# Optimization experiments

Measured on AMD Instinct MI355X. Metric: run time of the kernel, lower is better.

The kernel has to match this reference:

```python
import jax, jax.numpy as jnp
import numpy as np

B, H, S, D = 2, 16, 2048, 128


def setup_inputs() -> dict:
    key = jax.random.key(0)
    kq, kk, kv = jax.random.split(key, 3)
    q = jax.random.normal(kq, (B, H, S, D), dtype=jnp.float32)
    k = jax.random.normal(kk, (B, H, S, D), dtype=jnp.float32)
    v = jax.random.normal(kv, (B, H, S, D), dtype=jnp.float32)
    return {"q": q, "k": k, "v": v}


def reference(q, k, v):
    # cp_size == 1 path: causal scaled dot-product attention.
    # Identical math to the ring online-softmax accumulation collapsed to one step.
    d = q.shape[-1]
    scale = d ** -0.5
    scores = jnp.einsum("bhsd,bhtd->bhst", q, k) * scale  # (B,H,S,S)
    s = scores.shape[-1]
    causal_mask = jnp.tril(jnp.ones((s, s), dtype=bool))  # (S,S)
    scores = jnp.where(causal_mask, scores, -jnp.inf)
    probs = jax.nn.softmax(scores, axis=-1)
    return jnp.einsum("bhst,bhtd->bhsd", probs, v)
```

## Files before the change

### kernel.cpp

```cpp
#include <hip/hip_runtime.h>
#include <hip/hip_bf16.h>

constexpr int Bb = 2, Hh = 16, Ss = 2048, Dd = 128;
constexpr int BM = 64, BN = 64;
constexpr int NQT = Ss / BM;
constexpr float SCALE = 0.088388347648318447f * 1.4426950408889634f;

constexpr int KSTRIDE = 272;
constexpr int VSTRIDE = 144;

typedef __attribute__((ext_vector_type(8))) short bf16x8;
typedef __attribute__((ext_vector_type(4))) float f32x4;
typedef __attribute__((ext_vector_type(4))) int int4v;

__device__ __forceinline__ unsigned bfbits(float f) {
  union { float f; unsigned u; } v; v.f = f;
  return v.u + 0x7FFFu + ((v.u >> 16) & 1u);
}
__device__ __forceinline__ unsigned pkbf(float lo, float hi) {
#if __has_builtin(__builtin_amdgcn_cvt_pk_bf16_f32)
  typedef __attribute__((ext_vector_type(2))) __bf16 bf16x2;
  bf16x2 r = __builtin_amdgcn_cvt_pk_bf16_f32(lo, hi);
  return __builtin_bit_cast(unsigned, r);
#else
  return __builtin_amdgcn_perm(bfbits(hi), bfbits(lo), 0x07060302u);
#endif
}
__device__ __forceinline__ float exp2fast(float x) {
#if __has_builtin(__builtin_amdgcn_exp2f)
  return __builtin_amdgcn_exp2f(x);
#else
  return exp2f(x);
#endif
}
__device__ __forceinline__ float fcomp(float4 f, int j) {
  return j == 0 ? f.x : (j == 1 ? f.y : (j == 2 ? f.z : f.w));
}

__global__ __launch_bounds__(256, 3)
void fa_fwd_kernel(const float* __restrict__ q, const float* __restrict__ k,
                   const float* __restrict__ v, float* __restrict__ out) {
  __shared__ __align__(16) char Klds[BN * KSTRIDE];
  __shared__ __align__(16) char Vlds[Dd * VSTRIDE];

  const int tid = threadIdx.x;
  const int wave = tid >> 6, lane = tid & 63, quad = lane >> 4, l16 = lane & 15;
  const int bid = blockIdx.x;
  const int bh = bid & 31;
  const int qt = (NQT - 1) - (bid >> 5);

  const float* qb = q + (size_t)bh * Ss * Dd;
  const float* kb = k + (size_t)bh * Ss * Dd;
  const float* vb = v + (size_t)bh * Ss * Dd;

  bf16x8 qf[4];
  {
    const float* qr = qb + (size_t)(qt * BM + wave * 16 + l16) * Dd + quad * 8;
    #pragma unroll
    for (int ks = 0; ks < 4; ++ks) {
      float4 a = *(const float4*)(qr + ks * 32);
      float4 b = *(const float4*)(qr + ks * 32 + 4);
      int4v t = { (int)pkbf(a.x*SCALE, a.y*SCALE), (int)pkbf(a.z*SCALE, a.w*SCALE),
                  (int)pkbf(b.x*SCALE, b.y*SCALE), (int)pkbf(b.z*SCALE, b.w*SCALE) };
      qf[ks] = __builtin_bit_cast(bf16x8, t);
    }
  }

  const int krow0 = tid >> 4;
  const int kblk  = tid & 15;
  const int vdq = tid >> 3;
  const int vkg = tid & 7;

  float4 ka[4], kc[4];
  float4 vr[8];

  auto load_tiles = [&](int kt) {
    const float* Kg = kb + (size_t)(kt * BN) * Dd + kblk * 8;
    #pragma unroll
    for (int i = 0; i < 4; ++i) {
      ka[i] = *(const float4*)(Kg + (size_t)(krow0 + 16 * i) * Dd);
      kc[i] = *(const float4*)(Kg + (size_t)(krow0 + 16 * i) * Dd + 4);
    }
    const float* Vg = vb + (size_t)(kt * BN + vkg * 8) * Dd + vdq * 4;
    #pragma unroll
    for (int r = 0; r < 8; ++r)
      vr[r] = *(const float4*)(Vg + (size_t)r * Dd);
  };

  auto stage_tiles = [&]() {
    #pragma unroll
    for (int i = 0; i < 4; ++i) {
      int4v t = { (int)pkbf(ka[i].x, ka[i].y), (int)pkbf(ka[i].z, ka[i].w),
                  (int)pkbf(kc[i].x, kc[i].y), (int)pkbf(kc[i].z, kc[i].w) };
      *(int4v*)(Klds + (krow0 + 16 * i) * KSTRIDE + kblk * 16) = t;
    }
    #pragma unroll
    for (int j = 0; j < 4; ++j) {
      int d = vdq * 4 + j;
      int4v t = { (int)pkbf(fcomp(vr[0], j), fcomp(vr[1], j)),
                  (int)pkbf(fcomp(vr[2], j), fcomp(vr[3], j)),
                  (int)pkbf(fcomp(vr[4], j), fcomp(vr[5], j)),
                  (int)pkbf(fcomp(vr[6], j), fcomp(vr[7], j)) };
      *(int4v*)(Vlds + d * VSTRIDE + vkg * 16) = t;
    }
  };

  f32x4 o[8];
  #pragma unroll
  for (int i = 0; i < 8; ++i) o[i] = (f32x4)(0.0f);
  float mrow = -3.0e38f, lrow = 0.0f;

  load_tiles(0);
  stage_tiles();

  const int hi2 = quad >> 1;
  const int srcbase = (l16 + 32 * (quad & 1)) * 4;
  const char* Krd = Klds + l16 * KSTRIDE + quad * 16;
  const char* Vrd = Vlds + l16 * VSTRIDE + quad * 16;

  for (int kt = 0; kt <= qt; ++kt) {
    __syncthreads();
    const bool more = kt < qt;
    if (more) load_tiles(kt + 1);

    f32x4 acc[4];
    #pragma unroll
    for (int nt = 0; nt < 4; ++nt) acc[nt] = (f32x4)(0.0f);
    #pragma unroll
    for (int ks = 0; ks < 4; ++ks) {
      #pragma unroll
      for (int nt = 0; nt < 4; ++nt) {
        bf16x8 kf = *(const bf16x8*)(Krd + nt * (16 * KSTRIDE) + ks * 64);
        acc[nt] = __builtin_amdgcn_mfma_f32_16x16x32_bf16(kf, qf[ks], acc[nt], 0, 0, 0);
      }
    }

    if (kt == qt) {
      #pragma unroll
      for (int nt = 0; nt < 4; ++nt)
        #pragma unroll
        for (int r = 0; r < 4; ++r)
          if (nt * 16 + quad * 4 + r > wave * 16 + l16) acc[nt][r] = -1.0e30f;
    }

    float mx = acc[0][0];
    #pragma unroll
    for (int nt = 0; nt < 4; ++nt)
      #pragma unroll
      for (int r = 0; r < 4; ++r) mx = fmaxf(mx, acc[nt][r]);
    mx = fmaxf(mx, __shfl_xor(mx, 16, 64));
    mx = fmaxf(mx, __shfl_xor(mx, 32, 64));
    float mn = fmaxf(mrow, mx);
    float alpha = 1.0f;
    if (__any(mx > mrow)) {
      alpha = exp2fast(mrow - mn);
      #pragma unroll
      for (int r = 0; r < 4; ++r) {
        int src = (lane & 48) | (quad * 4 + r);
        float ar = __shfl(alpha, src, 64);
        #pragma unroll
        for (int dt = 0; dt < 8; ++dt) o[dt][r] *= ar;
      }
    }
    mrow = mn;
    float rs = 0.f;
    #pragma unroll
    for (int nt = 0; nt < 4; ++nt)
      #pragma unroll
      for (int r = 0; r < 4; ++r) {
        float p = exp2fast(acc[nt][r] - mn);
        acc[nt][r] = p; rs += p;
      }
    rs += __shfl_xor(rs, 16, 64);
    rs += __shfl_xor(rs, 32, 64);
    lrow = lrow * alpha + rs;

    unsigned pk0_0 = pkbf(acc[0][0], acc[0][1]), pk0_1 = pkbf(acc[0][2], acc[0][3]);
    unsigned pk1_0 = pkbf(acc[1][0], acc[1][1]), pk1_1 = pkbf(acc[1][2], acc[1][3]);
    unsigned pk2_0 = pkbf(acc[2][0], acc[2][1]), pk2_1 = pkbf(acc[2][2], acc[2][3]);
    unsigned pk3_0 = pkbf(acc[3][0], acc[3][1]), pk3_1 = pkbf(acc[3][2], acc[3][3]);

    bf16x8 pf[2];
    {
      int4v p0, p1;
      #pragma unroll
      for (int jp = 0; jp < 4; ++jp) {
        int srcb = srcbase + 64 * (jp >> 1);
        int a0 = __builtin_amdgcn_ds_bpermute(srcb, (int)((jp & 1) ? pk0_1 : pk0_0));
        int a1 = __builtin_amdgcn_ds_bpermute(srcb, (int)((jp & 1) ? pk1_1 : pk1_0));
        int a2 = __builtin_amdgcn_ds_bpermute(srcb, (int)((jp & 1) ? pk2_1 : pk2_0));
        int a3 = __builtin_amdgcn_ds_bpermute(srcb, (int)((jp & 1) ? pk3_1 : pk3_0));
        p0[jp] = hi2 ? a1 : a0;
        p1[jp] = hi2 ? a3 : a2;
      }
      pf[0] = __builtin_bit_cast(bf16x8, p0);
      pf[1] = __builtin_bit_cast(bf16x8, p1);
    }

    #pragma unroll
    for (int ks2 = 0; ks2 < 2; ++ks2) {
      #pragma unroll
      for (int dt = 0; dt < 8; ++dt) {
        bf16x8 vf = *(const bf16x8*)(Vrd + dt * (16 * VSTRIDE) + ks2 * 64);
        o[dt] = __builtin_amdgcn_mfma_f32_16x16x32_bf16(pf[ks2], vf, o[dt], 0, 0, 0);
      }
    }

    if (more) { __syncthreads(); stage_tiles(); }
  }

  float linv[4];
  #pragma unroll
  for (int r = 0; r < 4; ++r) {
    int src = (lane & 48) | (quad * 4 + r);
    linv[r] = 1.0f / __shfl(lrow, src, 64);
  }
  float* ob = out + ((size_t)bh * Ss + qt * BM + wave * 16) * Dd;
  #pragma unroll
  for (int dt = 0; dt < 8; ++dt)
    #pragma unroll
    for (int r = 0; r < 4; ++r)
      ob[(quad * 4 + r) * Dd + dt * 16 + l16] = o[dt][r] * linv[r];
}

extern "C" void kernel_launch(void* const* d_in, const int* in_sizes, int n_in,
                              void* d_out, int out_size, void* d_ws, size_t ws_size,
                              hipStream_t stream) {
  const float* q = (const float*)d_in[0];
  const float* k = (const float*)d_in[1];
  const float* v = (const float*)d_in[2];
  float* out = (float*)d_out;
  dim3 grid(Bb * Hh * NQT);
  dim3 block(256);
  hipLaunchKernelGGL(fa_fwd_kernel, grid, block, 0, stream, q, k, v, out);
}
```

Measured before the change: 214.8 us.

## Process two query sub-tiles per block with double-buffered LDS and permuted K rows

Each block now handles 128 query rows as two 64-row groups, so every K/V tile staged in LDS feeds twice as many MFMAs and global K/V traffic per query drops. LDS is double-buffered, which removes the second barrier before staging the next tile. K rows are stored in a permuted order so the QK^T accumulator layout matches the PV A-operand layout directly, replacing the ds_bpermute shuffles with plain packing. The trade-off is more registers and LDS per block (occupancy hint lowered from 3 to 2), half as many blocks, and coarser causal load balancing.

```diff
diff --git a/kernel.cpp b/kernel.cpp
--- a/kernel.cpp
+++ b/kernel.cpp
@@ -2,12 +2,14 @@
 #include <hip/hip_bf16.h>
 
 constexpr int Bb = 2, Hh = 16, Ss = 2048, Dd = 128;
-constexpr int BM = 64, BN = 64;
+constexpr int BM = 128, BN = 64;
 constexpr int NQT = Ss / BM;
 constexpr float SCALE = 0.088388347648318447f * 1.4426950408889634f;
 
 constexpr int KSTRIDE = 272;
 constexpr int VSTRIDE = 144;
+constexpr int KBYTES = BN * KSTRIDE;
+constexpr int VBYTES = Dd * VSTRIDE;
 
 typedef __attribute__((ext_vector_type(8))) short bf16x8;
 typedef __attribute__((ext_vector_type(4))) float f32x4;
@@ -36,33 +38,39 @@
 __device__ __forceinline__ float fcomp(float4 f, int j) {
   return j == 0 ? f.x : (j == 1 ? f.y : (j == 2 ? f.z : f.w));
 }
-
-__global__ __launch_bounds__(256, 3)
+__device__ __forceinline__ int permrow(int key) {
+  return ((key >> 5) & 1) * 16 + ((key >> 2) & 1) * 32 +
+         ((key >> 3) & 3) * 4 + (key & 3);
+}
+
+__global__ __launch_bounds__(256, 2)
 void fa_fwd_kernel(const float* __restrict__ q, const float* __restrict__ k,
                    const float* __restrict__ v, float* __restrict__ out) {
-  __shared__ __align__(16) char Klds[BN * KSTRIDE];
-  __shared__ __align__(16) char Vlds[Dd * VSTRIDE];
+  __shared__ __align__(16) char Klds[2 * KBYTES];
+  __shared__ __align__(16) char Vlds[2 * VBYTES];
 
   const int tid = threadIdx.x;
   const int wave = tid >> 6, lane = tid & 63, quad = lane >> 4, l16 = lane & 15;
   const int bid = blockIdx.x;
   const int bh = bid & 31;
-  const int qt = (NQT - 1) - (bid >> 5);
+  const int t = (NQT - 1) - (bid >> 5);
+  const int last = 2 * t + 1;
 
   const float* qb = q + (size_t)bh * Ss * Dd;
   const float* kb = k + (size_t)bh * Ss * Dd;
   const float* vb = v + (size_t)bh * Ss * Dd;
 
-  bf16x8 qf[4];
-  {
-    const float* qr = qb + (size_t)(qt * BM + wave * 16 + l16) * Dd + quad * 8;
+  bf16x8 qf[2][4];
+  #pragma unroll
+  for (int g = 0; g < 2; ++g) {
+    const float* qr = qb + (size_t)(t * BM + g * 64 + wave * 16 + l16) * Dd + quad * 8;
     #pragma unroll
     for (int ks = 0; ks < 4; ++ks) {
       float4 a = *(const float4*)(qr + ks * 32);
       float4 b = *(const float4*)(qr + ks * 32 + 4);
-      int4v t = { (int)pkbf(a.x*SCALE, a.y*SCALE), (int)pkbf(a.z*SCALE, a.w*SCALE),
-                  (int)pkbf(b.x*SCALE, b.y*SCALE), (int)pkbf(b.z*SCALE, b.w*SCALE) };
-      qf[ks] = __builtin_bit_cast(bf16x8, t);
+      int4v tt = { (int)pkbf(a.x*SCALE, a.y*SCALE), (int)pkbf(a.z*SCALE, a.w*SCALE),
+                   (int)pkbf(b.x*SCALE, b.y*SCALE), (int)pkbf(b.z*SCALE, b.w*SCALE) };
+      qf[g][ks] = __builtin_bit_cast(bf16x8, tt);
     }
   }
 
@@ -87,140 +95,151 @@
       vr[r] = *(const float4*)(Vg + (size_t)r * Dd);
   };
 
-  auto stage_tiles = [&]() {
+  auto stage_tiles = [&](int buf) {
+    char* Kst = Klds + buf * KBYTES;
+    char* Vst = Vlds + buf * VBYTES;
     #pragma unroll
     for (int i = 0; i < 4; ++i) {
-      int4v t = { (int)pkbf(ka[i].x, ka[i].y), (int)pkbf(ka[i].z, ka[i].w),
-                  (int)pkbf(kc[i].x, kc[i].y), (int)pkbf(kc[i].z, kc[i].w) };
-      *(int4v*)(Klds + (krow0 + 16 * i) * KSTRIDE + kblk * 16) = t;
+      int row = permrow(krow0 + 16 * i);
+      int4v tt = { (int)pkbf(ka[i].x, ka[i].y), (int)pkbf(ka[i].z, ka[i].w),
+                   (int)pkbf(kc[i].x, kc[i].y), (int)pkbf(kc[i].z, kc[i].w) };
+      *(int4v*)(Kst + row * KSTRIDE + kblk * 16) = tt;
     }
     #pragma unroll
     for (int j = 0; j < 4; ++j) {
       int d = vdq * 4 + j;
-      int4v t = { (int)pkbf(fcomp(vr[0], j), fcomp(vr[1], j)),
-                  (int)pkbf(fcomp(vr[2], j), fcomp(vr[3], j)),
-                  (int)pkbf(fcomp(vr[4], j), fcomp(vr[5], j)),
-                  (int)pkbf(fcomp(vr[6], j), fcomp(vr[7], j)) };
-      *(int4v*)(Vlds + d * VSTRIDE + vkg * 16) = t;
+      int4v tt = { (int)pkbf(fcomp(vr[0], j), fcomp(vr[1], j)),
+                   (int)pkbf(fcomp(vr[2], j), fcomp(vr[3], j)),
+                   (int)pkbf(fcomp(vr[4], j), fcomp(vr[5], j)),
+                   (int)pkbf(fcomp(vr[6], j), fcomp(vr[7], j)) };
+      *(int4v*)(Vst + d * VSTRIDE + vkg * 16) = tt;
     }
   };
 
-  f32x4 o[8];
+  f32x4 o[2][8];
   #pragma unroll
-  for (int i = 0; i < 8; ++i) o[i] = (f32x4)(0.0f);
-  float mrow = -3.0e38f, lrow = 0.0f;
+  for (int g = 0; g < 2; ++g)
+    #pragma unroll
+    for (int i = 0; i < 8; ++i) o[g][i] = (f32x4)(0.0f);
+  float mrow[2] = {-3.0e38f, -3.0e38f};
+  float lrow[2] = {0.0f, 0.0f};
 
   load_tiles(0);
-  stage_tiles();
-
-  const int hi2 = quad >> 1;
-  const int srcbase = (l16 + 32 * (quad & 1)) * 4;
-  const char* Krd = Klds + l16 * KSTRIDE + quad * 16;
-  const char* Vrd = Vlds + l16 * VSTRIDE + quad * 16;
-
-  for (int kt = 0; kt <= qt; ++kt) {
+  stage_tiles(0);
+
+  for (int kt = 0; kt <= last; ++kt) {
     __syncthreads();
-    const bool more = kt < qt;
+    const bool more = kt < last;
     if (more) load_tiles(kt + 1);
 
-    f32x4 acc[4];
-    #pragma unroll
-    for (int nt = 0; nt < 4; ++nt) acc[nt] = (f32x4)(0.0f);
+    const char* Krd = Klds + (kt & 1) * KBYTES + l16 * KSTRIDE + quad * 16;
+    const char* Vrd = Vlds + (kt & 1) * VBYTES + l16 * VSTRIDE + quad * 16;
+
+    f32x4 acc[2][4];
+    #pragma unroll
+    for (int g = 0; g < 2; ++g)
+      #pragma unroll
+      for (int nt = 0; nt < 4; ++nt) acc[g][nt] = (f32x4)(0.0f);
     #pragma unroll
     for (int ks = 0; ks < 4; ++ks) {
       #pragma unroll
       for (int nt = 0; nt < 4; ++nt) {
         bf16x8 kf = *(const bf16x8*)(Krd + nt * (16 * KSTRIDE) + ks * 64);
-        acc[nt] = __builtin_amdgcn_mfma_f32_16x16x32_bf16(kf, qf[ks], acc[nt], 0, 0, 0);
-      }
-    }
-
-    if (kt == qt) {
+        #pragma unroll
+        for (int g = 0; g < 2; ++g)
+          acc[g][nt] = __builtin_amdgcn_mfma_f32_16x16x32_bf16(kf, qf[g][ks], acc[g][nt], 0, 0, 0);
+      }
+    }
+
+    if (kt >= 2 * t) {
+      #pragma unroll
+      for (int g = 0; g < 2; ++g)
+        #pragma unroll
+        for (int nt = 0; nt < 4; ++nt)
+          #pragma unroll
+          for (int r = 0; r < 4; ++r) {
+            int key = 32 * (nt & 1) + 8 * quad + 4 * (nt >> 1) + r;
+            if (kt * 64 + key > t * BM + g * 64 + wave * 16 + l16)
+              acc[g][nt][r] = -1.0e30f;
+          }
+    }
+
+    #pragma unroll
+    for (int g = 0; g < 2; ++g) {
+      float mx = acc[g][0][0];
       #pragma unroll
       for (int nt = 0; nt < 4; ++nt)
         #pragma unroll
-        for (int r = 0; r < 4; ++r)
-          if (nt * 16 + quad * 4 + r > wave * 16 + l16) acc[nt][r] = -1.0e30f;
-    }
-
-    float mx = acc[0][0];
-    #pragma unroll
-    for (int nt = 0; nt < 4; ++nt)
-      #pragma unroll
-      for (int r = 0; r < 4; ++r) mx = fmaxf(mx, acc[nt][r]);
-    mx = fmaxf(mx, __shfl_xor(mx, 16, 64));
-    mx = fmaxf(mx, __shfl_xor(mx, 32, 64));
-    float mn = fmaxf(mrow, mx);
-    float alpha = 1.0f;
-    if (__any(mx > mrow)) {
-      alpha = exp2fast(mrow - mn);
-      #pragma unroll
-      for (int r = 0; r < 4; ++r) {
-        int src = (lane & 48) | (quad * 4 + r);
-        float ar = __shfl(alpha, src, 64);
-        #pragma unroll
-        for (int dt = 0; dt < 8; ++dt) o[dt][r] *= ar;
-      }
-    }
-    mrow = mn;
-    float rs = 0.f;
-    #pragma unroll
-    for (int nt = 0; nt < 4; ++nt)
-      #pragma unroll
-      for (int r = 0; r < 4; ++r) {
-        float p = exp2fast(acc[nt][r] - mn);
-        acc[nt][r] = p; rs += p;
-      }
-    rs += __shfl_xor(rs, 16, 64);
-    rs += __shfl_xor(rs, 32, 64);
-    lrow = lrow * alpha + rs;
-
-    unsigned pk0_0 = pkbf(acc[0][0], acc[0][1]), pk0_1 = pkbf(acc[0][2], acc[0][3]);
-    unsigned pk1_0 = pkbf(acc[1][0], acc[1][1]), pk1_1 = pkbf(acc[1][2], acc[1][3]);
-    unsigned pk2_0 = pkbf(acc[2][0], acc[2][1]), pk2_1 = pkbf(acc[2][2], acc[2][3]);
-    unsigned pk3_0 = pkbf(acc[3][0], acc[3][1]), pk3_1 = pkbf(acc[3][2], acc[3][3]);
-
-    bf16x8 pf[2];
-    {
-      int4v p0, p1;
-      #pragma unroll
-      for (int jp = 0; jp < 4; ++jp) {
-        int srcb = srcbase + 64 * (jp >> 1);
-        int a0 = __builtin_amdgcn_ds_bpermute(srcb, (int)((jp & 1) ? pk0_1 : pk0_0));
-        int a1 = __builtin_amdgcn_ds_bpermute(srcb, (int)((jp & 1) ? pk1_1 : pk1_0));
-        int a2 = __builtin_amdgcn_ds_bpermute(srcb, (int)((jp & 1) ? pk2_1 : pk2_0));
-        int a3 = __builtin_amdgcn_ds_bpermute(srcb, (int)((jp & 1) ? pk3_1 : pk3_0));
-        p0[jp] = hi2 ? a1 : a0;
-        p1[jp] = hi2 ? a3 : a2;
-      }
-      pf[0] = __builtin_bit_cast(bf16x8, p0);
-      pf[1] = __builtin_bit_cast(bf16x8, p1);
-    }
+        for (int r = 0; r < 4; ++r) mx = fmaxf(mx, acc[g][nt][r]);
+      mx = fmaxf(mx, __shfl_xor(mx, 16, 64));
+      mx = fmaxf(mx, __shfl_xor(mx, 32, 64));
+      float mn = fmaxf(mrow[g], mx);
+      float alpha = 1.0f;
+      if (__any(mx > mrow[g])) {
+        alpha = exp2fast(mrow[g] - mn);
+        #pragma unroll
+        for (int r = 0; r < 4; ++r) {
+          int src = (lane & 48) | (quad * 4 + r);
+          float ar = __shfl(alpha, src, 64);
+          #pragma unroll
+          for (int dt = 0; dt < 8; ++dt) o[g][dt][r] *= ar;
+        }
+      }
+      mrow[g] = mn;
+      float rs = 0.f;
+      #pragma unroll
+      for (int nt = 0; nt < 4; ++nt)
+        #pragma unroll
+        for (int r = 0; r < 4; ++r) {
+          float p = exp2fast(acc[g][nt][r] - mn);
+          acc[g][nt][r] = p; rs += p;
+        }
+      rs += __shfl_xor(rs, 16, 64);
+      rs += __shfl_xor(rs, 32, 64);
+      lrow[g] = lrow[g] * alpha + rs;
+    }
+
+    bf16x8 pf[2][2];
+    #pragma unroll
+    for (int g = 0; g < 2; ++g)
+      #pragma unroll
+      for (int ks2 = 0; ks2 < 2; ++ks2) {
+        int4v tt = { (int)pkbf(acc[g][ks2][0],     acc[g][ks2][1]),
+                     (int)pkbf(acc[g][ks2][2],     acc[g][ks2][3]),
+                     (int)pkbf(acc[g][ks2 + 2][0], acc[g][ks2 + 2][1]),
+                     (int)pkbf(acc[g][ks2 + 2][2], acc[g][ks2 + 2][3]) };
+        pf[g][ks2] = __builtin_bit_cast(bf16x8, tt);
+      }
 
     #pragma unroll
     for (int ks2 = 0; ks2 < 2; ++ks2) {
       #pragma unroll
       for (int dt = 0; dt < 8; ++dt) {
         bf16x8 vf = *(const bf16x8*)(Vrd + dt * (16 * VSTRIDE) + ks2 * 64);
-        o[dt] = __builtin_amdgcn_mfma_f32_16x16x32_bf16(pf[ks2], vf, o[dt], 0, 0, 0);
-      }
-    }
-
-    if (more) { __syncthreads(); stage_tiles(); }
+        #pragma unroll
+        for (int g = 0; g < 2; ++g)
+          o[g][dt] = __builtin_amdgcn_mfma_f32_16x16x32_bf16(pf[g][ks2], vf, o[g][dt], 0, 0, 0);
+      }
+    }
+
+    if (more) stage_tiles((kt + 1) & 1);
   }
 
-  float linv[4];
   #pragma unroll
-  for (int r = 0; r < 4; ++r) {
-    int src = (lane & 48) | (quad * 4 + r);
-    linv[r] = 1.0f / __shfl(lrow, src, 64);
+  for (int g = 0; g < 2; ++g) {
+    float linv[4];
+    #pragma unroll
+    for (int r = 0; r < 4; ++r) {
+      int src = (lane & 48) | (quad * 4 + r);
+      linv[r] = 1.0f / __shfl(lrow[g], src, 64);
+    }
+    float* ob = out + ((size_t)bh * Ss + t * BM + g * 64 + wave * 16) * Dd;
+    #pragma unroll
+    for (int dt = 0; dt < 8; ++dt)
+      #pragma unroll
+      for (int r = 0; r < 4; ++r)
+        ob[(quad * 4 + r) * Dd + dt * 16 + l16] = o[g][dt][r] * linv[r];
   }
-  float* ob = out + ((size_t)bh * Ss + qt * BM + wave * 16) * Dd;
-  #pragma unroll
-  for (int dt = 0; dt < 8; ++dt)
-    #pragma unroll
-    for (int r = 0; r < 4; ++r)
-      ob[(quad * 4 + r) * Dd + dt * 16 + l16] = o[dt][r] * linv[r];
 }
 
 extern "C" void kernel_launch(void* const* d_in, const int* in_sizes, int n_in,
```

Measured after the change: 223.8 us. +4.2%, slower.

## Permute K rows in LDS to drop P bpermute shuffles; rebalance causal tile order

Applied to the files above, without the earlier changes.

K rows are written into LDS in a permuted order, so each lane's S-tile accumulator already holds the keys it needs as the A operand of the PV MFMA. That removes the eight ds_bpermute ops and selects per iteration, and the causal mask is rewritten with the permuted key index to match. The launch bound occupancy target rises from 3 to 4 blocks per CU, which may add register pressure or spills. The query-tile schedule is reordered to interleave long and short causal tiles, aiming at better load balance across the grid.

```diff
diff --git a/kernel.cpp b/kernel.cpp
--- a/kernel.cpp
+++ b/kernel.cpp
@@ -36,8 +36,12 @@
 __device__ __forceinline__ float fcomp(float4 f, int j) {
   return j == 0 ? f.x : (j == 1 ? f.y : (j == 2 ? f.z : f.w));
 }
-
-__global__ __launch_bounds__(256, 3)
+__device__ __forceinline__ int permrow(int key) {
+  return ((key >> 5) & 1) * 16 + ((key >> 2) & 1) * 32 +
+         ((key >> 3) & 3) * 4 + (key & 3);
+}
+
+__global__ __launch_bounds__(256, 4)
 void fa_fwd_kernel(const float* __restrict__ q, const float* __restrict__ k,
                    const float* __restrict__ v, float* __restrict__ out) {
   __shared__ __align__(16) char Klds[BN * KSTRIDE];
@@ -47,7 +51,9 @@
   const int wave = tid >> 6, lane = tid & 63, quad = lane >> 4, l16 = lane & 15;
   const int bid = blockIdx.x;
   const int bh = bid & 31;
-  const int qt = (NQT - 1) - (bid >> 5);
+  const int s = bid >> 5;
+  const int qt = (s < 8) ? (31 - s) : (s < 16) ? (s - 8)
+               : (s < 24) ? (39 - s) : (s - 16);
 
   const float* qb = q + (size_t)bh * Ss * Dd;
   const float* kb = k + (size_t)bh * Ss * Dd;
@@ -90,9 +96,10 @@
   auto stage_tiles = [&]() {
     #pragma unroll
     for (int i = 0; i < 4; ++i) {
+      int row = permrow(krow0 + 16 * i);
       int4v t = { (int)pkbf(ka[i].x, ka[i].y), (int)pkbf(ka[i].z, ka[i].w),
                   (int)pkbf(kc[i].x, kc[i].y), (int)pkbf(kc[i].z, kc[i].w) };
-      *(int4v*)(Klds + (krow0 + 16 * i) * KSTRIDE + kblk * 16) = t;
+      *(int4v*)(Klds + row * KSTRIDE + kblk * 16) = t;
     }
     #pragma unroll
     for (int j = 0; j < 4; ++j) {
@@ -113,8 +120,6 @@
   load_tiles(0);
   stage_tiles();
 
-  const int hi2 = quad >> 1;
-  const int srcbase = (l16 + 32 * (quad & 1)) * 4;
   const char* Krd = Klds + l16 * KSTRIDE + quad * 16;
   const char* Vrd = Vlds + l16 * VSTRIDE + quad * 16;
 
@@ -139,8 +144,10 @@
       #pragma unroll
       for (int nt = 0; nt < 4; ++nt)
         #pragma unroll
-        for (int r = 0; r < 4; ++r)
-          if (nt * 16 + quad * 4 + r > wave * 16 + l16) acc[nt][r] = -1.0e30f;
+        for (int r = 0; r < 4; ++r) {
+          int key = 32 * (nt & 1) + 8 * quad + 4 * (nt >> 1) + r;
+          if (key > wave * 16 + l16) acc[nt][r] = -1.0e30f;
+        }
     }
 
     float mx = acc[0][0];
@@ -175,26 +182,14 @@
     rs += __shfl_xor(rs, 32, 64);
     lrow = lrow * alpha + rs;
 
-    unsigned pk0_0 = pkbf(acc[0][0], acc[0][1]), pk0_1 = pkbf(acc[0][2], acc[0][3]);
-    unsigned pk1_0 = pkbf(acc[1][0], acc[1][1]), pk1_1 = pkbf(acc[1][2], acc[1][3]);
-    unsigned pk2_0 = pkbf(acc[2][0], acc[2][1]), pk2_1 = pkbf(acc[2][2], acc[2][3]);
-    unsigned pk3_0 = pkbf(acc[3][0], acc[3][1]), pk3_1 = pkbf(acc[3][2], acc[3][3]);
-
     bf16x8 pf[2];
-    {
-      int4v p0, p1;
-      #pragma unroll
-      for (int jp = 0; jp < 4; ++jp) {
-        int srcb = srcbase + 64 * (jp >> 1);
-        int a0 = __builtin_amdgcn_ds_bpermute(srcb, (int)((jp & 1) ? pk0_1 : pk0_0));
-        int a1 = __builtin_amdgcn_ds_bpermute(srcb, (int)((jp & 1) ? pk1_1 : pk1_0));
-        int a2 = __builtin_amdgcn_ds_bpermute(srcb, (int)((jp & 1) ? pk2_1 : pk2_0));
-        int a3 = __builtin_amdgcn_ds_bpermute(srcb, (int)((jp & 1) ? pk3_1 : pk3_0));
-        p0[jp] = hi2 ? a1 : a0;
-        p1[jp] = hi2 ? a3 : a2;
-      }
-      pf[0] = __builtin_bit_cast(bf16x8, p0);
-      pf[1] = __builtin_bit_cast(bf16x8, p1);
+    #pragma unroll
+    for (int ks2 = 0; ks2 < 2; ++ks2) {
+      int4v t = { (int)pkbf(acc[ks2][0],     acc[ks2][1]),
+                  (int)pkbf(acc[ks2][2],     acc[ks2][3]),
+                  (int)pkbf(acc[ks2 + 2][0], acc[ks2 + 2][1]),
+                  (int)pkbf(acc[ks2 + 2][2], acc[ks2 + 2][3]) };
+      pf[ks2] = __builtin_bit_cast(bf16x8, t);
     }
 
     #pragma unroll
```

Measured after the change: 401.4 us. 86.9% more time.
